# Kernel optimization log

Measured on AMD Instinct MI355X. Metric: run time of the kernel, lower is better.

Reference implementation:

```python
import jax, jax.numpy as jnp
import numpy as np

D_MODEL = 1024
D_STATE = 16
D_CONV = 4
EXPAND = 2
D_INNER = EXPAND * D_MODEL          # 2048
DT_RANK = (D_MODEL + 15) // 16      # 64
BSZ, T0, H0, W0 = 4, 8, 16, 16
SEQLEN = T0 * H0 * W0               # 2048
N_BANDS = 8


def setup_inputs() -> dict:
    key = jax.random.key(0)
    ks = jax.random.split(key, 8)
    hidden_states = jax.random.normal(ks[0], (BSZ, SEQLEN, D_MODEL), jnp.float32)
    in_proj_w = jax.random.normal(ks[1], (2 * D_INNER, D_MODEL), jnp.float32) * (D_MODEL ** -0.5)
    conv_w = jax.random.normal(ks[2], (D_INNER, 1, D_CONV), jnp.float32) * (D_CONV ** -0.5)
    conv_b = jnp.zeros((D_INNER,), jnp.float32)
    x_proj_w = jax.random.normal(ks[3], (DT_RANK + 2 * D_STATE, D_INNER), jnp.float32) * (D_INNER ** -0.5)
    dt_std = DT_RANK ** -0.5
    dt_proj_w = jax.random.uniform(ks[4], (D_INNER, DT_RANK), jnp.float32, -dt_std, dt_std)
    # inverse-softplus init of dt bias, as in the torch module
    dt = jnp.exp(jax.random.uniform(ks[5], (D_INNER,), jnp.float32)
                 * (np.log(0.1) - np.log(0.001)) + np.log(0.001))
    dt = jnp.clip(dt, 1e-4, None)
    dt_proj_b = dt + jnp.log(-jnp.expm1(-dt))
    A_log = jnp.log(jnp.tile(jnp.arange(1, D_STATE + 1, dtype=jnp.float32)[None, :], (D_INNER, 1)))
    D_param = jnp.ones((D_INNER,), jnp.float32)
    out_proj_w = jax.random.normal(ks[6], (D_MODEL, D_INNER), jnp.float32) * (D_INNER ** -0.5)
    return dict(hidden_states=hidden_states, T=T0, H=H0, W=W0,
                in_proj_w=in_proj_w, conv_w=conv_w, conv_b=conv_b,
                x_proj_w=x_proj_w, dt_proj_w=dt_proj_w, dt_proj_b=dt_proj_b,
                A_log=A_log, D=D_param, out_proj_w=out_proj_w)


def _channel_alignment(x, B, T, H, W):
    """x: (B, C, L=T*H*W) -> (align_loss scalar, features (B*T, C))."""
    C = x.shape[1]
    x4 = x.reshape(B, C, T, H, W).transpose(0, 2, 1, 3, 4).reshape(B * T, C, H, W)
    fr = jnp.fft.rfft2(x4, axes=(-2, -1))
    mag = jnp.sqrt(fr.real ** 2 + fr.imag ** 2 + 1e-8)
    mag = jnp.fft.fftshift(mag, axes=(-2, -1))
    Wr = mag.shape[-1]                      # W//2 + 1
    hg = jnp.arange(H)[:, None]
    wg = jnp.arange(Wr)[None, :]
    r = jnp.sqrt(((hg - H // 2) / H) ** 2 + ((wg - Wr // 2) / Wr) ** 2)
    masks = jnp.stack([((r >= i / N_BANDS) & (r < (i + 1) / N_BANDS)).astype(mag.dtype)
                       for i in range(N_BANDS)])          # (8, H, Wr)
    bands = jnp.einsum('bchw,khw->bck', mag, masks)        # (B*T, C, 8)
    bands = bands / (bands.sum(-1, keepdims=True) + 1e-8)
    features = bands[..., N_BANDS // 2:].sum(-1)           # (B*T, C) high-freq ratio
    fn = features / jnp.maximum(jnp.linalg.norm(features, axis=1, keepdims=True), 1e-12)
    sim = fn @ fn.T
    Bt = features.shape[0]
    loss = 1.0 - sim.sum() / (Bt * Bt)
    return loss, features


def _invert_A(A_log, features):
    """Blend A_log toward its column-flipped version, weighted by channel features."""
    A_max = A_log.max(axis=0, keepdims=True)
    A_min = A_log.min(axis=0, keepdims=True)
    A_flipped = A_max + A_min - A_log
    attention = jnp.linalg.norm(jnp.exp(A_log), axis=1)
    attention = attention / (attention.max() + 1e-8)
    f = jax.nn.softmax(jax.lax.stop_gradient(features).mean(axis=0))
    alpha = jnp.clip(f * (1.0 - attention), 0.0, 1.0)[:, None]   # (d_inner, 1)
    return (1.0 - alpha) * A_log + alpha * A_flipped


def reference(hidden_states, T, H, W, in_proj_w, conv_w, conv_b,
              x_proj_w, dt_proj_w, dt_proj_b, A_log, D, out_proj_w):
    B, L, _ = hidden_states.shape
    xz = jnp.einsum('bld,ed->bel', hidden_states, in_proj_w)      # (B, 2*d_inner, L)
    x, z = xz[:, :D_INNER], xz[:, D_INNER:]

    align_loss, features = _channel_alignment(x, B, T, H, W)
    A_log_new = _invert_A(A_log, features)
    A = -jnp.exp(A_log_new)                                       # (d_inner, d_state)

    # causal depthwise conv1d + SiLU (left pad d_conv-1 == torch pad then slice :L)
    xc = jax.lax.conv_general_dilated(x, conv_w, (1,), [(D_CONV - 1, 0)],
                                      dimension_numbers=('NCH', 'OIH', 'NCH'),
                                      feature_group_count=D_INNER)
    xc = jax.nn.silu(xc + conv_b[None, :, None])                  # (B, d_inner, L)

    x_dbl = jnp.einsum('bdl,ed->ble', xc, x_proj_w)               # (B, L, dt_rank+2N)
    dt_low = x_dbl[..., :DT_RANK]
    Bm = x_dbl[..., DT_RANK:DT_RANK + D_STATE]                    # (B, L, N)
    Cm = x_dbl[..., DT_RANK + D_STATE:]                           # (B, L, N)
    delta = jax.nn.softplus(jnp.einsum('blr,dr->bld', dt_low, dt_proj_w) + dt_proj_b)

    u = xc.transpose(0, 2, 1)                                     # (B, L, d_inner)

    def step(s, inp):
        d_t, u_t, B_t, C_t = inp                                  # (B,D),(B,D),(B,N),(B,N)
        s = s * jnp.exp(d_t[..., None] * A) + (d_t * u_t)[..., None] * B_t[:, None, :]
        y_t = jnp.einsum('bdn,bn->bd', s, C_t)
        return s, y_t

    s0 = jnp.zeros((B, D_INNER, D_STATE), delta.dtype)
    _, ys = jax.lax.scan(step, s0,
                         (delta.transpose(1, 0, 2), u.transpose(1, 0, 2),
                          Bm.transpose(1, 0, 2), Cm.transpose(1, 0, 2)))
    y = ys.transpose(1, 0, 2)                                     # (B, L, d_inner)
    y = y + u * D
    y = y * jax.nn.silu(z.transpose(0, 2, 1))
    out = jnp.einsum('bld,ed->ble', y, out_proj_w)                # (B, L, d_model)
    return out, align_loss
```

## Files before the change

kernel.cpp:

```cpp
#include <hip/hip_runtime.h>
#include <math.h>
#include <stdint.h>

#define LSEQ 2048
#define DM   1024
#define DI   2048
#define NC   32
#define CL   64

#define OFF_X     ((size_t)0)
#define OFF_Z     ((size_t)16777216)
#define OFF_U     ((size_t)33554432)
#define OFF_S     ((size_t)50331648)
#define OFF_CS    (OFF_S)
#define OFF_SDT   (OFF_S + 4194304)
#define OFF_XDBL  (OFF_S + 4456448)
#define OFF_FEAT  (OFF_S + 5242880)
#define OFF_AWS   (OFF_S + 5308448)
#define OFF_B1    ((size_t)58720256)

__device__ __forceinline__ float silu_(float x) { return x / (1.f + __expf(-x)); }
__device__ __forceinline__ float softplus_(float x) {
  return fmaxf(x, 0.f) + log1pf(__expf(-fabsf(x)));
}
__device__ __forceinline__ unsigned short f2bf(float x) {
  unsigned int u = __float_as_uint(x);
  u += 0x7fffu + ((u >> 16) & 1u);
  return (unsigned short)(u >> 16);
}
__device__ __forceinline__ float bf2f(unsigned short h) {
  return __uint_as_float(((unsigned int)h) << 16);
}

typedef __attribute__((ext_vector_type(8))) short bf16x8;
typedef __attribute__((ext_vector_type(4))) float f32x4;

__device__ __forceinline__ void gl2lds16(const void* g, void* l) {
  __builtin_amdgcn_global_load_lds(
      (const __attribute__((address_space(1))) unsigned int*)(uintptr_t)g,
      (__attribute__((address_space(3))) unsigned int*)(uintptr_t)l,
      16, 0, 0);
}

#define BARRIER_()                                   \
  do {                                               \
    asm volatile("" ::: "memory");                   \
    __builtin_amdgcn_s_barrier();                    \
    asm volatile("" ::: "memory");                   \
  } while (0)

__global__ __launch_bounds__(256) void split2_w(
    const float* __restrict__ a, unsigned short* __restrict__ oa, int ksa,
    size_t na4,
    const float* __restrict__ b, unsigned short* __restrict__ ob, int ksb)
{
  size_t i4 = ((size_t)blockIdx.x << 8) + threadIdx.x;
  const float* src; unsigned short* dst; int ks;
  if (i4 < na4) { src = a; dst = oa; ks = ksa; }
  else          { src = b; dst = ob; ks = ksb; i4 -= na4; }
  const size_t flat = i4 << 2;
  const int K = 1 << ks;
  const size_t row = flat >> ks;
  const int k = (int)(flat & (size_t)(K - 1));
  float4 v = *(const float4*)(src + flat);
  float f[4] = {v.x, v.y, v.z, v.w};
  unsigned short h[4], lo[4];
#pragma unroll
  for (int c = 0; c < 4; ++c) { h[c] = f2bf(f[c]); lo[c] = f2bf(f[c] - bf2f(h[c])); }
  unsigned short* o = dst + (row << (ks + 1)) + k;
  *(uint2*)(o)     = make_uint2((unsigned)h[0]  | ((unsigned)h[1]  << 16),
                                (unsigned)h[2]  | ((unsigned)h[3]  << 16));
  *(uint2*)(o + K) = make_uint2((unsigned)lo[0] | ((unsigned)lo[1] << 16),
                                (unsigned)lo[2] | ((unsigned)lo[3] << 16));
}

template <int NPASS, int MH, int NH>
__device__ __forceinline__ void phase_mfma(
    const unsigned short* __restrict__ shc, f32x4 (&acc)[8][4],
    int wm, int wn, int lm, int roff)
{
  bf16x8 aH[4], bH[2], aL[4], bL[2];
#pragma unroll
  for (int ii = 0; ii < 4; ++ii) {
    const int ar = (wm + (MH * 4 + ii) * 16 + lm) * 32 + roff;
    aH[ii] = *(const bf16x8*)(shc + ar);
    if constexpr (NPASS > 1) aL[ii] = *(const bf16x8*)(shc + 2 * 8192 + ar);
  }
#pragma unroll
  for (int jj = 0; jj < 2; ++jj) {
    const int br = (wn + (NH * 2 + jj) * 16 + lm) * 32 + roff;
    bH[jj] = *(const bf16x8*)(shc + 8192 + br);
    if constexpr (NPASS > 1) bL[jj] = *(const bf16x8*)(shc + 3 * 8192 + br);
  }
  __builtin_amdgcn_s_setprio(1);
#pragma unroll
  for (int ii = 0; ii < 4; ++ii)
#pragma unroll
    for (int jj = 0; jj < 2; ++jj) {
      const int i = MH * 4 + ii, j = NH * 2 + jj;
      acc[i][j] = __builtin_amdgcn_mfma_f32_16x16x32_bf16(aH[ii], bH[jj], acc[i][j], 0, 0, 0);
      if constexpr (NPASS > 1) {
        acc[i][j] = __builtin_amdgcn_mfma_f32_16x16x32_bf16(aH[ii], bL[jj], acc[i][j], 0, 0, 0);
        acc[i][j] = __builtin_amdgcn_mfma_f32_16x16x32_bf16(aL[ii], bH[jj], acc[i][j], 0, 0, 0);
      }
    }
  __builtin_amdgcn_s_setprio(0);
}

template <int NPASS>
__global__ __launch_bounds__(512, 2) void gemm_8ph(
    const unsigned short* __restrict__ Ap, const unsigned short* __restrict__ Bp,
    float* __restrict__ C, int K, int ldc)
{
  constexpr int NTEN = (NPASS > 1) ? 4 : 2;
  __shared__ unsigned short sh[2][NTEN][256 * 32];
  const int tid = threadIdx.x;
  const int bn = blockIdx.x << 8;
  const int bm = blockIdx.y << 8;
  const int K2 = K * 2;
  const int wave = tid >> 6, lane = tid & 63;
  const int wm = (wave >> 2) << 7;
  const int wn = (wave & 3) << 6;
  const int lm = lane & 15, quad = lane >> 4;
  const int roff = ((quad ^ ((lm >> 1) & 3)) << 3);

  const int r0 = tid >> 2;
  const int kq = (((tid & 3) ^ ((r0 >> 1) & 3)) << 3);
  const unsigned short* a0 = Ap + (size_t)(bm + r0) * K2 + kq;
  const unsigned short* a1 = a0 + (size_t)128 * K2;
  const unsigned short* b0 = Bp + (size_t)(bn + r0) * K2 + kq;
  const unsigned short* b1 = b0 + (size_t)128 * K2;
  const int ls0 = tid * 8, ls1 = 4096 + tid * 8;

  f32x4 acc[8][4] = {};
  const int NT = K >> 5;

  {
    unsigned short* s = &sh[0][0][0];
    gl2lds16(a0, s + ls0);
    gl2lds16(a1, s + ls1);
    if constexpr (NPASS > 1) {
      gl2lds16(a0 + K, s + 2 * 8192 + ls0);
      gl2lds16(a1 + K, s + 2 * 8192 + ls1);
    }
    gl2lds16(b0, s + 8192 + ls0);
    gl2lds16(b1, s + 8192 + ls1);
    if constexpr (NPASS > 1) {
      gl2lds16(b0 + K, s + 3 * 8192 + ls0);
      gl2lds16(b1 + K, s + 3 * 8192 + ls1);
    }
  }

  for (int t = 0; t < NT - 1; ++t) {
    const unsigned short* cur = &sh[t & 1][0][0];
    unsigned short* nxt = &sh[(t + 1) & 1][0][0];
    const int kn = (t + 1) << 5;

    gl2lds16(a0 + kn, nxt + ls0);
    gl2lds16(a1 + kn, nxt + ls1);
    if constexpr (NPASS > 1) {
      gl2lds16(a0 + K + kn, nxt + 2 * 8192 + ls0);
      gl2lds16(a1 + K + kn, nxt + 2 * 8192 + ls1);
      asm volatile("s_waitcnt vmcnt(4)" ::: "memory");
    } else {
      asm volatile("s_waitcnt vmcnt(2)" ::: "memory");
    }
    BARRIER_();
    phase_mfma<NPASS, 0, 0>(cur, acc, wm, wn, lm, roff);
    BARRIER_();
    gl2lds16(b0 + kn, nxt + 8192 + ls0);
    gl2lds16(b1 + kn, nxt + 8192 + ls1);
    if constexpr (NPASS > 1) {
      gl2lds16(b0 + K + kn, nxt + 3 * 8192 + ls0);
      gl2lds16(b1 + K + kn, nxt + 3 * 8192 + ls1);
    }
    phase_mfma<NPASS, 0, 1>(cur, acc, wm, wn, lm, roff);
    BARRIER_();
    phase_mfma<NPASS, 1, 0>(cur, acc, wm, wn, lm, roff);
    BARRIER_();
    phase_mfma<NPASS, 1, 1>(cur, acc, wm, wn, lm, roff);
    BARRIER_();
  }

  {
    const unsigned short* cur = &sh[(NT - 1) & 1][0][0];
    asm volatile("s_waitcnt vmcnt(0)" ::: "memory");
    BARRIER_();
    phase_mfma<NPASS, 0, 0>(cur, acc, wm, wn, lm, roff);
    BARRIER_();
    phase_mfma<NPASS, 0, 1>(cur, acc, wm, wn, lm, roff);
    BARRIER_();
    phase_mfma<NPASS, 1, 0>(cur, acc, wm, wn, lm, roff);
    BARRIER_();
    phase_mfma<NPASS, 1, 1>(cur, acc, wm, wn, lm, roff);
  }

#pragma unroll
  for (int i = 0; i < 8; ++i) {
    const int m = bm + wm + i * 16 + quad * 4;
#pragma unroll
    for (int j = 0; j < 4; ++j) {
      const int n = bn + wn + j * 16 + lm;
#pragma unroll
      for (int r = 0; r < 4; ++r)
        C[(size_t)(m + r) * ldc + n] = acc[i][j][r];
    }
  }
}

template <int MH>
__device__ __forceinline__ void phaseM8(
    const unsigned short* __restrict__ ah, const unsigned short* __restrict__ al,
    const unsigned short* __restrict__ bh, const unsigned short* __restrict__ bl,
    f32x4 (&acc)[8][2], int wm, int wn, int lm, int roff)
{
  bf16x8 aH[4], aL[4], bH[2], bL[2];
#pragma unroll
  for (int ii = 0; ii < 4; ++ii) {
    const int ar = (wm + (MH * 4 + ii) * 16 + lm) * 32 + roff;
    aH[ii] = *(const bf16x8*)(ah + ar);
    aL[ii] = *(const bf16x8*)(al + ar);
  }
#pragma unroll
  for (int jj = 0; jj < 2; ++jj) {
    const int br = (wn + jj * 16 + lm) * 32 + roff;
    bH[jj] = *(const bf16x8*)(bh + br);
    bL[jj] = *(const bf16x8*)(bl + br);
  }
  __builtin_amdgcn_s_setprio(1);
#pragma unroll
  for (int ii = 0; ii < 4; ++ii)
#pragma unroll
    for (int jj = 0; jj < 2; ++jj) {
      const int i = MH * 4 + ii;
      acc[i][jj] = __builtin_amdgcn_mfma_f32_16x16x32_bf16(aH[ii], bH[jj], acc[i][jj], 0, 0, 0);
      acc[i][jj] = __builtin_amdgcn_mfma_f32_16x16x32_bf16(aH[ii], bL[jj], acc[i][jj], 0, 0, 0);
      acc[i][jj] = __builtin_amdgcn_mfma_f32_16x16x32_bf16(aL[ii], bH[jj], acc[i][jj], 0, 0, 0);
    }
  __builtin_amdgcn_s_setprio(0);
}

__global__ __launch_bounds__(512, 2) void gemm8_8ph(
    const unsigned int* __restrict__ Ay,
    const unsigned short* __restrict__ Bp,
    float* __restrict__ C)
{
  constexpr int K = 2048, K2 = 4096, ldc = 1024, NT = 64;
  __shared__ unsigned short AHs[2][256 * 32];
  __shared__ unsigned short ALs[2][256 * 32];
  __shared__ unsigned short BHs[2][128 * 32];
  __shared__ unsigned short BLs[2][128 * 32];
  const int tid = threadIdx.x;
  const int bn = blockIdx.x << 7;
  const int bm = blockIdx.y << 8;
  const int wave = tid >> 6, lane = tid & 63;
  const int wm = (wave >> 2) << 7;
  const int wn = (wave & 3) << 5;
  const int lm = lane & 15, quad = lane >> 4;
  const int roff = ((quad ^ ((lm >> 1) & 3)) << 3);

  const int ra = tid >> 1;
  const int g0 = (tid & 1) << 1;
  const int aswz = (ra >> 1) & 3;
  const int sa0 = (ra * 32) + ((g0 ^ aswz) << 3);
  const int sa1 = (ra * 32) + (((g0 + 1) ^ aswz) << 3);
  const unsigned int* ag = Ay + (size_t)(bm + ra) * K + (g0 << 3);

  const int rb = tid >> 2;
  const int kqb = (((tid & 3) ^ ((rb >> 1) & 3)) << 3);
  const unsigned short* bg = Bp + (size_t)(bn + rb) * K2 + kqb;
  const int lsb = tid * 8;

  f32x4 acc[8][2] = {};
  uint4 r0a, r0b, r0c, r0d, r1a, r1b, r1c, r1d;

#define LOADA_(d0, d1, d2, d3, kn) do {                                   \
    const uint4* p_ = (const uint4*)(ag + (kn));                          \
    d0 = p_[0]; d1 = p_[1]; d2 = p_[2]; d3 = p_[3]; } while (0)
#define WRITEA_(bufi, w0, w1, w2, w3) do {                                \
    unsigned h0 = (w0.x & 0xffffu) | (w0.y << 16);                        \
    unsigned h1 = (w0.z & 0xffffu) | (w0.w << 16);                        \
    unsigned h2 = (w1.x & 0xffffu) | (w1.y << 16);                        \
    unsigned h3 = (w1.z & 0xffffu) | (w1.w << 16);                        \
    unsigned h4 = (w2.x & 0xffffu) | (w2.y << 16);                        \
    unsigned h5 = (w2.z & 0xffffu) | (w2.w << 16);                        \
    unsigned h6 = (w3.x & 0xffffu) | (w3.y << 16);                        \
    unsigned h7 = (w3.z & 0xffffu) | (w3.w << 16);                        \
    unsigned l0 = (w0.x >> 16) | (w0.y & 0xffff0000u);                    \
    unsigned l1 = (w0.z >> 16) | (w0.w & 0xffff0000u);                    \
    unsigned l2 = (w1.x >> 16) | (w1.y & 0xffff0000u);                    \
    unsigned l3 = (w1.z >> 16) | (w1.w & 0xffff0000u);                    \
    unsigned l4 = (w2.x >> 16) | (w2.y & 0xffff0000u);                    \
    unsigned l5 = (w2.z >> 16) | (w2.w & 0xffff0000u);                    \
    unsigned l6 = (w3.x >> 16) | (w3.y & 0xffff0000u);                    \
    unsigned l7 = (w3.z >> 16) | (w3.w & 0xffff0000u);                    \
    *(uint4*)&AHs[bufi][sa0] = make_uint4(h0, h1, h2, h3);                \
    *(uint4*)&AHs[bufi][sa1] = make_uint4(h4, h5, h6, h7);                \
    *(uint4*)&ALs[bufi][sa0] = make_uint4(l0, l1, l2, l3);                \
    *(uint4*)&ALs[bufi][sa1] = make_uint4(l4, l5, l6, l7); } while (0)

#define BODY_(t, Ca, Cb, Cc, Cd, Na, Nb_, Nc, Nd, cb, nb) do {            \
    LOADA_(Ca, Cb, Cc, Cd, ((t) + 2) << 5);                               \
    gl2lds16(bg + (((t) + 1) << 5),     &BHs[nb][lsb]);                   \
    gl2lds16(bg + K + (((t) + 1) << 5), &BLs[nb][lsb]);                   \
    asm volatile("s_waitcnt vmcnt(6)" ::: "memory");                      \
    BARRIER_();                                                           \
    phaseM8<0>(AHs[cb], ALs[cb], BHs[cb], BLs[cb], acc, wm, wn, lm, roff);\
    BARRIER_();                                                           \
    WRITEA_(nb, Na, Nb_, Nc, Nd);                                         \
    phaseM8<1>(AHs[cb], ALs[cb], BHs[cb], BLs[cb], acc, wm, wn, lm, roff);\
    asm volatile("s_waitcnt lgkmcnt(0)" ::: "memory");                    \
    BARRIER_();                                                           \
  } while (0)

  LOADA_(r0a, r0b, r0c, r0d, 0);
  gl2lds16(bg,     &BHs[0][lsb]);
  gl2lds16(bg + K, &BLs[0][lsb]);
  LOADA_(r1a, r1b, r1c, r1d, 32);
  asm volatile("s_waitcnt vmcnt(4)" ::: "memory");
  WRITEA_(0, r0a, r0b, r0c, r0d);
  asm volatile("s_waitcnt lgkmcnt(0)" ::: "memory");
  BARRIER_();

  for (int t = 0; t + 3 < NT; t += 2) {
    BODY_(t,     r0a, r0b, r0c, r0d, r1a, r1b, r1c, r1d, 0, 1);
    BODY_(t + 1, r1a, r1b, r1c, r1d, r0a, r0b, r0c, r0d, 1, 0);
  }

  gl2lds16(bg + ((NT - 1) << 5),     &BHs[1][lsb]);
  gl2lds16(bg + K + ((NT - 1) << 5), &BLs[1][lsb]);
  asm volatile("s_waitcnt vmcnt(2)" ::: "memory");
  BARRIER_();
  phaseM8<0>(AHs[0], ALs[0], BHs[0], BLs[0], acc, wm, wn, lm, roff);
  BARRIER_();
  WRITEA_(1, r1a, r1b, r1c, r1d);
  phaseM8<1>(AHs[0], ALs[0], BHs[0], BLs[0], acc, wm, wn, lm, roff);
  asm volatile("s_waitcnt lgkmcnt(0)" ::: "memory");
  BARRIER_();
  asm volatile("s_waitcnt vmcnt(0)" ::: "memory");
  BARRIER_();
  phaseM8<0>(AHs[1], ALs[1], BHs[1], BLs[1], acc, wm, wn, lm, roff);
  BARRIER_();
  phaseM8<1>(AHs[1], ALs[1], BHs[1], BLs[1], acc, wm, wn, lm, roff);

#undef LOADA_
#undef WRITEA_
#undef BODY_

#pragma unroll
  for (int i = 0; i < 8; ++i) {
    const int m = bm + wm + i * 16 + quad * 4;
#pragma unroll
    for (int j = 0; j < 2; ++j) {
      const int n = bn + wn + j * 16 + lm;
#pragma unroll
      for (int r = 0; r < 4; ++r)
        C[(size_t)(m + r) * ldc + n] = acc[i][j][r];
    }
  }
}

template <int EPI>
__global__ __launch_bounds__(256) void gemm_nt(
    const float* __restrict__ A, int lda,
    const float* __restrict__ B, int ldb,
    float* __restrict__ C, int ldc,
    int N, int K, const float* __restrict__ bias, size_t cseg)
{
  __shared__ float As[16][68];
  __shared__ float Bs[16][68];
  const int tid = threadIdx.x;
  const int bm = blockIdx.y << 6;
  const int bn = blockIdx.x << 6;
  const int kz = blockIdx.z;
  A += (size_t)kz * K;
  B += (size_t)kz * K;
  C += (size_t)kz * cseg;
  const int lr = tid >> 2;
  const int lk = (tid & 3) << 2;
  const int tx = tid & 15, ty = tid >> 4;

  float acc[4][4];
#pragma unroll
  for (int i = 0; i < 4; ++i)
#pragma unroll
    for (int j = 0; j < 4; ++j) acc[i][j] = 0.f;

  const float* Apt = A + (size_t)(bm + lr) * lda + lk;
  const float* Bpt = B + (size_t)(bn + lr) * ldb + lk;
  const bool bv = (bn + lr) < N;

  for (int k0 = 0; k0 < K; k0 += 16) {
    float4 a4 = *(const float4*)(Apt + k0);
    float4 b4 = bv ? *(const float4*)(Bpt + k0) : make_float4(0.f, 0.f, 0.f, 0.f);
    __syncthreads();
    As[lk + 0][lr] = a4.x; As[lk + 1][lr] = a4.y;
    As[lk + 2][lr] = a4.z; As[lk + 3][lr] = a4.w;
    Bs[lk + 0][lr] = b4.x; Bs[lk + 1][lr] = b4.y;
    Bs[lk + 2][lr] = b4.z; Bs[lk + 3][lr] = b4.w;
    __syncthreads();
#pragma unroll
    for (int k = 0; k < 16; ++k) {
      const float4 av = *(const float4*)(&As[k][ty << 2]);
      const float4 bw = *(const float4*)(&Bs[k][tx << 2]);
      float a4r[4] = {av.x, av.y, av.z, av.w};
      float b4r[4] = {bw.x, bw.y, bw.z, bw.w};
#pragma unroll
      for (int i = 0; i < 4; ++i)
#pragma unroll
        for (int j = 0; j < 4; ++j)
          acc[i][j] = fmaf(a4r[i], b4r[j], acc[i][j]);
    }
  }

  const int m = bm + (ty << 2);
  const int n = bn + (tx << 2);
#pragma unroll
  for (int i = 0; i < 4; ++i) {
    float v[4] = {acc[i][0], acc[i][1], acc[i][2], acc[i][3]};
    if (EPI == 1) {
#pragma unroll
      for (int j = 0; j < 4; ++j)
        if (n + j < N) v[j] = softplus_(v[j] + bias[n + j]);
    }
    if (n + 3 < N) {
      *(float4*)(C + (size_t)(m + i) * ldc + n) = make_float4(v[0], v[1], v[2], v[3]);
    } else {
#pragma unroll
      for (int j = 0; j < 4; ++j)
        if (n + j < N) C[(size_t)(m + i) * ldc + n + j] = v[j];
    }
  }
}

__global__ __launch_bounds__(256) void reduce4(
    const float* __restrict__ P, float* __restrict__ O, size_t seg)
{
  const size_t i = ((size_t)blockIdx.x << 8) + threadIdx.x;
  float4 a = ((const float4*)P)[i];
  float4 b = ((const float4*)(P + seg))[i];
  float4 c = ((const float4*)(P + 2 * seg))[i];
  float4 d = ((const float4*)(P + 3 * seg))[i];
  ((float4*)O)[i] = make_float4(a.x + b.x + c.x + d.x,
                                a.y + b.y + c.y + d.y,
                                a.z + b.z + c.z + d.z,
                                a.w + b.w + c.w + d.w);
}

__global__ __launch_bounds__(256) void feat_kernel(
    const float* __restrict__ X, float* __restrict__ features)
{
  __shared__ float xin[256][17];
  __shared__ float Rf[16 * 315];
  __shared__ float tc[16], ts[16];
  __shared__ float part2[16][16][2];

  const int tid = threadIdx.x;
  const int frame = blockIdx.x >> 7;
  const int cg = blockIdx.x & 127;
  const int b = frame >> 3, t = frame & 7;
  const int c0 = cg << 4;

  if (tid < 16) {
    float ang = 0.39269908169872414f * (float)tid;
    tc[tid] = cosf(ang);
    ts[tid] = sinf(ang);
  }
  const float* xb = X + ((size_t)(b * LSEQ + t * 256) << 11) + c0;
  for (int i = tid; i < 256 * 16; i += 256) {
    int hw = i >> 4, ci = i & 15;
    xin[hw][ci] = xb[((size_t)hw << 11) + ci];
  }
  __syncthreads();

  {
    const int ci = tid & 15, h = tid >> 4;
    float re[9], im[9];
#pragma unroll
    for (int kw = 0; kw < 9; ++kw) { re[kw] = 0.f; im[kw] = 0.f; }
#pragma unroll
    for (int w = 0; w < 16; ++w) {
      float x = xin[(h << 4) + w][ci];
#pragma unroll
      for (int kw = 0; kw < 9; ++kw) {
        int ph = (kw * w) & 15;
        re[kw] = fmaf(x, tc[ph], re[kw]);
        im[kw] = fmaf(-x, ts[ph], im[kw]);
      }
    }
#pragma unroll
    for (int kw = 0; kw < 9; ++kw) {
      Rf[ci * 315 + kw * 35 + 2 * h]     = re[kw];
      Rf[ci * 315 + kw * 35 + 2 * h + 1] = im[kw];
    }
  }
  __syncthreads();

  {
    const int ci = tid & 15, kh = tid >> 4;
    float ut = 0.f, tt = 0.f;
    for (int kw = 0; kw < 9; ++kw) {
      float fre = 0.f, fim = 0.f;
#pragma unroll
      for (int h = 0; h < 16; ++h) {
        int ph = (kh * h) & 15;
        float c = tc[ph], s = ts[ph];
        float rr = Rf[ci * 315 + kw * 35 + 2 * h];
        float ri = Rf[ci * 315 + kw * 35 + 2 * h + 1];
        fre += rr * c + ri * s;
        fim += ri * c - rr * s;
      }
      float mag = sqrtf(fre * fre + fim * fim + 1e-8f);
      int sh = (kh + 8) & 15;
      int sw2 = kw + 4; if (sw2 >= 9) sw2 -= 9;
      float dh = (float)(sh - 8) / 16.0f;
      float dw = (float)(sw2 - 4) / 9.0f;
      tt += mag;
      if (dh * dh + dw * dw >= 0.25f) ut += mag;
    }
    part2[ci][kh][0] = ut;
    part2[ci][kh][1] = tt;
  }
  __syncthreads();

  if (tid < 16) {
    float ut = 0.f, tt = 0.f;
    for (int kh = 0; kh < 16; ++kh) { ut += part2[tid][kh][0]; tt += part2[tid][kh][1]; }
    features[frame * DI + c0 + tid] = ut / (tt + 1e-8f);
  }
}

__global__ __launch_bounds__(256) void alpha_kernel(
    const float* __restrict__ feats, const float* __restrict__ A_log,
    float* __restrict__ Aws, float* __restrict__ loss_out)
{
  __shared__ float red[256];
  __shared__ float invn[32];
  __shared__ float PT[32][257];
  __shared__ float AM[256][17];
  __shared__ float sAmax[16], sAmin[16];
  const int tid = threadIdx.x;

  float pn[32];
#pragma unroll
  for (int i = 0; i < 32; ++i) pn[i] = 0.f;
  float md[8];
#pragma unroll
  for (int j = 0; j < 8; ++j) md[j] = 0.f;
  for (int i = 0; i < 32; ++i) {
#pragma unroll
    for (int j = 0; j < 8; ++j) {
      float v = feats[(i << 11) + tid + (j << 8)];
      pn[i] = fmaf(v, v, pn[i]);
      md[j] += v;
    }
  }
#pragma unroll
  for (int j = 0; j < 8; ++j) md[j] *= (1.f / 32.f);
#pragma unroll
  for (int i = 0; i < 32; ++i) PT[i][tid] = pn[i];
  __syncthreads();
  if (tid < 32) {
    float s = 0.f;
    for (int k = 0; k < 256; ++k) s += PT[tid][k];
    invn[tid] = 1.f / fmaxf(sqrtf(s), 1e-12f);
  }
  __syncthreads();

  float gsq = 0.f;
#pragma unroll
  for (int j = 0; j < 8; ++j) {
    float gd = 0.f;
    for (int i = 0; i < 32; ++i)
      gd = fmaf(feats[(i << 11) + tid + (j << 8)], invn[i], gd);
    gsq = fmaf(gd, gd, gsq);
  }
  red[tid] = gsq; __syncthreads();
  for (int s = 128; s > 0; s >>= 1) { if (tid < s) red[tid] += red[tid + s]; __syncthreads(); }
  if (tid == 0) loss_out[0] = 1.f - red[0] * (1.f / 1024.f);
  __syncthreads();

  float lm = md[0];
#pragma unroll
  for (int j = 1; j < 8; ++j) lm = fmaxf(lm, md[j]);
  red[tid] = lm; __syncthreads();
  for (int s = 128; s > 0; s >>= 1) { if (tid < s) red[tid] = fmaxf(red[tid], red[tid + s]); __syncthreads(); }
  const float mmax = red[0]; __syncthreads();

  float p[8]; float ps = 0.f;
#pragma unroll
  for (int j = 0; j < 8; ++j) { p[j] = __expf(md[j] - mmax); ps += p[j]; }
  red[tid] = ps; __syncthreads();
  for (int s = 128; s > 0; s >>= 1) { if (tid < s) red[tid] += red[tid + s]; __syncthreads(); }
  const float psum = red[0]; __syncthreads();

  float amaxl[16], aminl[16], rn[8];
#pragma unroll
  for (int n = 0; n < 16; ++n) { amaxl[n] = -1e30f; aminl[n] = 1e30f; }
#pragma unroll
  for (int j = 0; j < 8; ++j) {
    const int d = tid + (j << 8);
    float ss = 0.f;
#pragma unroll
    for (int n = 0; n < 16; ++n) {
      float a = A_log[(d << 4) + n];
      float e = __expf(a);
      ss = fmaf(e, e, ss);
      amaxl[n] = fmaxf(amaxl[n], a);
      aminl[n] = fminf(aminl[n], a);
    }
    rn[j] = sqrtf(ss);
  }
  float rm = rn[0];
#pragma unroll
  for (int j = 1; j < 8; ++j) rm = fmaxf(rm, rn[j]);
  red[tid] = rm; __syncthreads();
  for (int s = 128; s > 0; s >>= 1) { if (tid < s) red[tid] = fmaxf(red[tid], red[tid + s]); __syncthreads(); }
  const float rnmax = red[0]; __syncthreads();

#pragma unroll
  for (int n = 0; n < 16; ++n) AM[tid][n] = amaxl[n];
  __syncthreads();
  if (tid < 16) { float m = -1e30f; for (int i = 0; i < 256; ++i) m = fmaxf(m, AM[i][tid]); sAmax[tid] = m; }
  __syncthreads();
#pragma unroll
  for (int n = 0; n < 16; ++n) AM[tid][n] = aminl[n];
  __syncthreads();
  if (tid < 16) { float m = 1e30f; for (int i = 0; i < 256; ++i) m = fminf(m, AM[i][tid]); sAmin[tid] = m; }
  __syncthreads();

  const float irn = 1.f / (rnmax + 1e-8f);
#pragma unroll
  for (int j = 0; j < 8; ++j) {
    const int d = tid + (j << 8);
    const float att = rn[j] * irn;
    const float f = p[j] / psum;
    const float alpha = fminf(fmaxf(f * (1.f - att), 0.f), 1.f);
#pragma unroll
    for (int n = 0; n < 16; ++n) {
      float a = A_log[(d << 4) + n];
      float fl = sAmax[n] + sAmin[n] - a;
      float an = (1.f - alpha) * a + alpha * fl;
      Aws[(d << 4) + n] = -__expf(an) * 1.4426950408889634f;
    }
  }
}

__global__ __launch_bounds__(256) void conv_kernel(
    const float* __restrict__ X, const float* __restrict__ cw,
    const float* __restrict__ cb, float* __restrict__ U)
{
  const size_t i4 = ((size_t)blockIdx.x << 8) + threadIdx.x;
  const int e4 = (int)(i4 & 511);
  const size_t row = i4 >> 9;
  const int l = (int)(row & 2047);
  const float* xr = X + (row << 11) + (e4 << 2);
  const float4 z4 = make_float4(0.f, 0.f, 0.f, 0.f);
  float4 x0 = *(const float4*)xr;
  float4 x1 = (l >= 1) ? *(const float4*)(xr - 2048) : z4;
  float4 x2 = (l >= 2) ? *(const float4*)(xr - 4096) : z4;
  float4 x3 = (l >= 3) ? *(const float4*)(xr - 6144) : z4;
  const float4* cwf = (const float4*)cw;
  float4 bi = *(const float4*)(cb + (e4 << 2));
  float x0a[4] = {x0.x, x0.y, x0.z, x0.w};
  float x1a[4] = {x1.x, x1.y, x1.z, x1.w};
  float x2a[4] = {x2.x, x2.y, x2.z, x2.w};
  float x3a[4] = {x3.x, x3.y, x3.z, x3.w};
  float bia[4] = {bi.x, bi.y, bi.z, bi.w};
  float o[4];
#pragma unroll
  for (int c = 0; c < 4; ++c) {
    float4 w = cwf[(e4 << 2) + c];
    float acc = bia[c];
    acc = fmaf(x3a[c], w.x, acc);
    acc = fmaf(x2a[c], w.y, acc);
    acc = fmaf(x1a[c], w.z, acc);
    acc = fmaf(x0a[c], w.w, acc);
    o[c] = silu_(acc);
  }
  *(float4*)(U + (i4 << 2)) = make_float4(o[0], o[1], o[2], o[3]);
}

__global__ __launch_bounds__(256) void scan_pass1(
    const float* __restrict__ delta, const float* __restrict__ U,
    const float* __restrict__ xdbl, const float* __restrict__ Aws,
    float* __restrict__ cs, float* __restrict__ sdt)
{
  __shared__ float blds[CL * 16];
  const int tid = threadIdx.x;
  const int dg = blockIdx.x & 7;
  const int chunk = (blockIdx.x >> 3) & 31;
  const int b = blockIdx.x >> 8;
  const int d = (dg << 8) | tid;
  const int l0 = chunk * CL;

  for (int i = tid; i < CL * 16; i += 256) {
    int l = i >> 4, j = i & 15;
    blds[i] = xdbl[(size_t)(b * LSEQ + l0 + l) * 96 + 64 + j];
  }
  __syncthreads();

  float Ar[16];
#pragma unroll
  for (int n = 0; n < 16; ++n) Ar[n] = Aws[(d << 4) + n];
  float s[16];
#pragma unroll
  for (int n = 0; n < 16; ++n) s[n] = 0.f;
  float sumdt = 0.f;

  const float* dp = delta + ((size_t)b << 22) + ((size_t)l0 << 11) + d;
  const float* up = U + ((size_t)b << 22) + ((size_t)l0 << 11) + d;

  for (int l = 0; l < CL; ++l) {
    const float dt = dp[(size_t)l << 11];
    const float u = up[(size_t)l << 11];
    sumdt += dt;
    const float du = dt * u;
    const float* bl = &blds[l << 4];
#pragma unroll
    for (int n = 0; n < 16; ++n)
      s[n] = fmaf(s[n], __builtin_amdgcn_exp2f(dt * Ar[n]), du * bl[n]);
  }

  float* csp = cs + ((((size_t)b * NC + chunk) * 2048 + d) << 4);
#pragma unroll
  for (int n = 0; n < 4; ++n)
    *(float4*)(csp + (n << 2)) = make_float4(s[4*n], s[4*n+1], s[4*n+2], s[4*n+3]);
  sdt[((size_t)b * NC + chunk) * 2048 + d] = sumdt;
}

__global__ __launch_bounds__(256) void scan_mid(
    float* __restrict__ cs, const float* __restrict__ sdt,
    const float* __restrict__ Aws)
{
  const int b = blockIdx.x >> 3;
  const int d = ((blockIdx.x & 7) << 8) | threadIdx.x;
  float Ar[16];
#pragma unroll
  for (int n = 0; n < 16; ++n) Ar[n] = Aws[(d << 4) + n];
  float si[16];
#pragma unroll
  for (int n = 0; n < 16; ++n) si[n] = 0.f;

  for (int c = 0; c < NC; ++c) {
    const size_t base = ((size_t)b * NC + c) * 2048 + d;
    float* csp = cs + (base << 4);
    float sl[16];
#pragma unroll
    for (int n = 0; n < 4; ++n) {
      float4 v = *(const float4*)(csp + (n << 2));
      sl[4*n] = v.x; sl[4*n+1] = v.y; sl[4*n+2] = v.z; sl[4*n+3] = v.w;
    }
    const float sm = sdt[base];
#pragma unroll
    for (int n = 0; n < 4; ++n)
      *(float4*)(csp + (n << 2)) = make_float4(si[4*n], si[4*n+1], si[4*n+2], si[4*n+3]);
#pragma unroll
    for (int n = 0; n < 16; ++n)
      si[n] = fmaf(si[n], __builtin_amdgcn_exp2f(sm * Ar[n]), sl[n]);
  }
}

__global__ __launch_bounds__(256) void scan_pass3(
    const float* __restrict__ delta, const float* __restrict__ Z,
    float* __restrict__ U,
    const float* __restrict__ xdbl, const float* __restrict__ Aws,
    const float* __restrict__ Dp, const float* __restrict__ cs)
{
  __shared__ float bclds[CL * 32];
  const int tid = threadIdx.x;
  const int dg = blockIdx.x & 7;
  const int chunk = (blockIdx.x >> 3) & 31;
  const int b = blockIdx.x >> 8;
  const int d = (dg << 8) | tid;
  const int l0 = chunk * CL;

  for (int i = tid; i < CL * 32; i += 256) {
    int l = i >> 5, j = i & 31;
    bclds[i] = xdbl[(size_t)(b * LSEQ + l0 + l) * 96 + 64 + j];
  }
  __syncthreads();

  float Ar[16];
#pragma unroll
  for (int n = 0; n < 16; ++n) Ar[n] = Aws[(d << 4) + n];
  const float Dd = Dp[d];

  const float* csp = cs + ((((size_t)b * NC + chunk) * 2048 + d) << 4);
  float s[16];
#pragma unroll
  for (int n = 0; n < 4; ++n) {
    float4 v = *(const float4*)(csp + (n << 2));
    s[4*n] = v.x; s[4*n+1] = v.y; s[4*n+2] = v.z; s[4*n+3] = v.w;
  }

  const float* dp = delta + ((size_t)b << 22) + ((size_t)l0 << 11) + d;
  const float* zp = Z + ((size_t)b << 22) + ((size_t)l0 << 11) + d;
  float* up = U + ((size_t)b << 22) + ((size_t)l0 << 11) + d;

  for (int l = 0; l < CL; ++l) {
    const float dt = dp[(size_t)l << 11];
    const float u = up[(size_t)l << 11];
    const float z = zp[(size_t)l << 11];
    const float du = dt * u;
    const float* bcl = &bclds[l << 5];
    float y = 0.f;
#pragma unroll
    for (int n = 0; n < 16; ++n) {
      s[n] = fmaf(s[n], __builtin_amdgcn_exp2f(dt * Ar[n]), du * bcl[n]);
      y = fmaf(s[n], bcl[16 + n], y);
    }
    const float yv = fmaf(u, Dd, y);
    const float yo = yv * silu_(z);
    const unsigned short h = f2bf(yo);
    const unsigned short lo = f2bf(yo - bf2f(h));
    ((unsigned int*)up)[(size_t)l << 11] = (unsigned)h | ((unsigned)lo << 16);
  }
}

extern "C" void kernel_launch(void* const* d_in, const int* in_sizes, int n_in,
                              void* d_out, int out_size, void* d_ws, size_t ws_size,
                              hipStream_t stream)
{
  const float* hs         = (const float*)d_in[0];
  const float* in_proj_w  = (const float*)d_in[4];
  const float* conv_w     = (const float*)d_in[5];
  const float* conv_b     = (const float*)d_in[6];
  const float* x_proj_w   = (const float*)d_in[7];
  const float* dt_proj_w  = (const float*)d_in[8];
  const float* dt_proj_b  = (const float*)d_in[9];
  const float* A_log      = (const float*)d_in[10];
  const float* Dp         = (const float*)d_in[11];
  const float* out_proj_w = (const float*)d_in[12];
  float* out = (float*)d_out;
  float* ws = (float*)d_ws;

  float* X     = ws + OFF_X;
  float* Z     = ws + OFF_Z;
  float* U     = ws + OFF_U;
  float* cs    = ws + OFF_CS;
  float* sdt   = ws + OFF_SDT;
  float* xdbl  = ws + OFF_XDBL;
  float* feats = ws + OFF_FEAT;
  float* Aws   = ws + OFF_AWS;
  unsigned short* A1s = (unsigned short*)(ws + OFF_S);
  unsigned short* B1s = (unsigned short*)(ws + OFF_B1);
  unsigned short* B2s = (unsigned short*)(ws + OFF_B1);

  const dim3 blk(256);

  split2_w<<<12288, blk, 0, stream>>>(hs, A1s, 10, (size_t)2097152,
                                      in_proj_w, B1s, 10);
  gemm_8ph<3><<<dim3(8, 32), dim3(512), 0, stream>>>(A1s, B1s, X, 1024, 2048);
  gemm_8ph<1><<<dim3(8, 32), dim3(512), 0, stream>>>(A1s, B1s + (size_t)2048 * 2048, Z, 1024, 2048);
  feat_kernel<<<4096, blk, 0, stream>>>(X, feats);
  conv_kernel<<<16384, blk, 0, stream>>>(X, conv_w, conv_b, U);
  split2_w<<<2048, blk, 0, stream>>>(out_proj_w, B2s, 11, (size_t)524288,
                                     out_proj_w, B2s, 11);
  alpha_kernel<<<1, blk, 0, stream>>>(feats, A_log, Aws, out + 8388608);
  gemm_nt<0><<<dim3(2, 128, 4), blk, 0, stream>>>(U, DI, x_proj_w, DI, cs, 96, 96, 512, nullptr, (size_t)786432);
  reduce4<<<768, blk, 0, stream>>>(cs, xdbl, (size_t)786432);
  gemm_nt<1><<<dim3(32, 128, 1), blk, 0, stream>>>(xdbl, 96, dt_proj_w, 64, X, DI, DI, 64, dt_proj_b, 0);
  scan_pass1<<<1024, blk, 0, stream>>>(X, U, xdbl, Aws, cs, sdt);
  scan_mid<<<32, blk, 0, stream>>>(cs, sdt, Aws);
  scan_pass3<<<1024, blk, 0, stream>>>(X, Z, U, xdbl, Aws, Dp, cs);
  gemm8_8ph<<<dim3(8, 32), dim3(512), 0, stream>>>((const unsigned int*)U, B2s, out);
}
```

Before: 900.2 us.

## Stage packed A tile via direct global-to-LDS loads and split hi/lo at read

```diff
diff --git a/kernel.cpp b/kernel.cpp
--- a/kernel.cpp
+++ b/kernel.cpp
@@ -209,21 +209,34 @@
 }
 
 template <int MH>
-__device__ __forceinline__ void phaseM8(
-    const unsigned short* __restrict__ ah, const unsigned short* __restrict__ al,
+__device__ __forceinline__ void phase_pk(
+    const unsigned int* __restrict__ ap,
     const unsigned short* __restrict__ bh, const unsigned short* __restrict__ bl,
-    f32x4 (&acc)[8][2], int wm, int wn, int lm, int roff)
+    f32x4 (&acc)[8][2], int wm, int wn, int lm, int quad, int roffB)
 {
   bf16x8 aH[4], aL[4], bH[2], bL[2];
 #pragma unroll
   for (int ii = 0; ii < 4; ++ii) {
-    const int ar = (wm + (MH * 4 + ii) * 16 + lm) * 32 + roff;
-    aH[ii] = *(const bf16x8*)(ah + ar);
-    aL[ii] = *(const bf16x8*)(al + ar);
+    const int r = wm + (MH * 4 + ii) * 16 + lm;
+    const int s0 = (2 * quad) ^ (r & 7);
+    const int s1 = (2 * quad + 1) ^ (r & 7);
+    const uint4 w0 = *(const uint4*)(ap + ((size_t)(r * 8 + s0) << 2));
+    const uint4 w1 = *(const uint4*)(ap + ((size_t)(r * 8 + s1) << 2));
+    union { unsigned u[4]; bf16x8 v; } ch, cl;
+    ch.u[0] = __byte_perm(w0.x, w0.y, 0x5410u);
+    ch.u[1] = __byte_perm(w0.z, w0.w, 0x5410u);
+    ch.u[2] = __byte_perm(w1.x, w1.y, 0x5410u);
+    ch.u[3] = __byte_perm(w1.z, w1.w, 0x5410u);
+    cl.u[0] = __byte_perm(w0.x, w0.y, 0x7632u);
+    cl.u[1] = __byte_perm(w0.z, w0.w, 0x7632u);
+    cl.u[2] = __byte_perm(w1.x, w1.y, 0x7632u);
+    cl.u[3] = __byte_perm(w1.z, w1.w, 0x7632u);
+    aH[ii] = ch.v;
+    aL[ii] = cl.v;
   }
 #pragma unroll
   for (int jj = 0; jj < 2; ++jj) {
-    const int br = (wn + jj * 16 + lm) * 32 + roff;
+    const int br = (wn + jj * 16 + lm) * 32 + roffB;
     bH[jj] = *(const bf16x8*)(bh + br);
     bL[jj] = *(const bf16x8*)(bl + br);
   }
@@ -240,14 +253,13 @@
   __builtin_amdgcn_s_setprio(0);
 }
 
-__global__ __launch_bounds__(512, 2) void gemm8_8ph(
+__global__ __launch_bounds__(512, 2) void gemm8_pk(
     const unsigned int* __restrict__ Ay,
     const unsigned short* __restrict__ Bp,
     float* __restrict__ C)
 {
   constexpr int K = 2048, K2 = 4096, ldc = 1024, NT = 64;
-  __shared__ unsigned short AHs[2][256 * 32];
-  __shared__ unsigned short ALs[2][256 * 32];
+  __shared__ unsigned int   APk[2][2048 * 4];
   __shared__ unsigned short BHs[2][128 * 32];
   __shared__ unsigned short BLs[2][128 * 32];
   const int tid = threadIdx.x;
@@ -257,14 +269,11 @@
   const int wm = (wave >> 2) << 7;
   const int wn = (wave & 3) << 5;
   const int lm = lane & 15, quad = lane >> 4;
-  const int roff = ((quad ^ ((lm >> 1) & 3)) << 3);
-
-  const int ra = tid >> 1;
-  const int g0 = (tid & 1) << 1;
-  const int aswz = (ra >> 1) & 3;
-  const int sa0 = (ra * 32) + ((g0 ^ aswz) << 3);
-  const int sa1 = (ra * 32) + (((g0 + 1) ^ aswz) << 3);
-  const unsigned int* ag = Ay + (size_t)(bm + ra) * K + (g0 << 3);
+  const int roffB = ((quad ^ ((lm >> 1) & 3)) << 3);
+
+  const int ar0 = tid >> 3;
+  const int au = (tid & 7) ^ (ar0 & 7);
+  const unsigned int* ag = Ay + (size_t)(bm + ar0) * K + (au << 2);
 
   const int rb = tid >> 2;
   const int kqb = (((tid & 3) ^ ((rb >> 1) & 3)) << 3);
@@ -272,80 +281,38 @@
   const int lsb = tid * 8;
 
   f32x4 acc[8][2] = {};
-  uint4 r0a, r0b, r0c, r0d, r1a, r1b, r1c, r1d;
-
-#define LOADA_(d0, d1, d2, d3, kn) do {                                   \
-    const uint4* p_ = (const uint4*)(ag + (kn));                          \
-    d0 = p_[0]; d1 = p_[1]; d2 = p_[2]; d3 = p_[3]; } while (0)
-#define WRITEA_(bufi, w0, w1, w2, w3) do {                                \
-    unsigned h0 = (w0.x & 0xffffu) | (w0.y << 16);                        \
-    unsigned h1 = (w0.z & 0xffffu) | (w0.w << 16);                        \
-    unsigned h2 = (w1.x & 0xffffu) | (w1.y << 16);                        \
-    unsigned h3 = (w1.z & 0xffffu) | (w1.w << 16);                        \
-    unsigned h4 = (w2.x & 0xffffu) | (w2.y << 16);                        \
-    unsigned h5 = (w2.z & 0xffffu) | (w2.w << 16);                        \
-    unsigned h6 = (w3.x & 0xffffu) | (w3.y << 16);                        \
-    unsigned h7 = (w3.z & 0xffffu) | (w3.w << 16);                        \
-    unsigned l0 = (w0.x >> 16) | (w0.y & 0xffff0000u);                    \
-    unsigned l1 = (w0.z >> 16) | (w0.w & 0xffff0000u);                    \
-    unsigned l2 = (w1.x >> 16) | (w1.y & 0xffff0000u);                    \
-    unsigned l3 = (w1.z >> 16) | (w1.w & 0xffff0000u);                    \
-    unsigned l4 = (w2.x >> 16) | (w2.y & 0xffff0000u);                    \
-    unsigned l5 = (w2.z >> 16) | (w2.w & 0xffff0000u);                    \
-    unsigned l6 = (w3.x >> 16) | (w3.y & 0xffff0000u);                    \
-    unsigned l7 = (w3.z >> 16) | (w3.w & 0xffff0000u);                    \
-    *(uint4*)&AHs[bufi][sa0] = make_uint4(h0, h1, h2, h3);                \
-    *(uint4*)&AHs[bufi][sa1] = make_uint4(h4, h5, h6, h7);                \
-    *(uint4*)&ALs[bufi][sa0] = make_uint4(l0, l1, l2, l3);                \
-    *(uint4*)&ALs[bufi][sa1] = make_uint4(l4, l5, l6, l7); } while (0)
-
-#define BODY_(t, Ca, Cb, Cc, Cd, Na, Nb_, Nc, Nd, cb, nb) do {            \
-    LOADA_(Ca, Cb, Cc, Cd, ((t) + 2) << 5);                               \
-    gl2lds16(bg + (((t) + 1) << 5),     &BHs[nb][lsb]);                   \
-    gl2lds16(bg + K + (((t) + 1) << 5), &BLs[nb][lsb]);                   \
-    asm volatile("s_waitcnt vmcnt(6)" ::: "memory");                      \
-    BARRIER_();                                                           \
-    phaseM8<0>(AHs[cb], ALs[cb], BHs[cb], BLs[cb], acc, wm, wn, lm, roff);\
-    BARRIER_();                                                           \
-    WRITEA_(nb, Na, Nb_, Nc, Nd);                                         \
-    phaseM8<1>(AHs[cb], ALs[cb], BHs[cb], BLs[cb], acc, wm, wn, lm, roff);\
-    asm volatile("s_waitcnt lgkmcnt(0)" ::: "memory");                    \
-    BARRIER_();                                                           \
+
+#define STAGE_(buf, kn) do {                                                   \
+    gl2lds16(ag + (kn),                  &APk[buf][((size_t)(0 * 512 + tid)) << 2]); \
+    gl2lds16(ag + (size_t)64  * K + (kn), &APk[buf][((size_t)(1 * 512 + tid)) << 2]); \
+    gl2lds16(ag + (size_t)128 * K + (kn), &APk[buf][((size_t)(2 * 512 + tid)) << 2]); \
+    gl2lds16(ag + (size_t)192 * K + (kn), &APk[buf][((size_t)(3 * 512 + tid)) << 2]); \
+    gl2lds16(bg + (kn),     &BHs[buf][lsb]);                                   \
+    gl2lds16(bg + K + (kn), &BLs[buf][lsb]);                                   \
   } while (0)
 
-  LOADA_(r0a, r0b, r0c, r0d, 0);
-  gl2lds16(bg,     &BHs[0][lsb]);
-  gl2lds16(bg + K, &BLs[0][lsb]);
-  LOADA_(r1a, r1b, r1c, r1d, 32);
-  asm volatile("s_waitcnt vmcnt(4)" ::: "memory");
-  WRITEA_(0, r0a, r0b, r0c, r0d);
-  asm volatile("s_waitcnt lgkmcnt(0)" ::: "memory");
-  BARRIER_();
-
-  for (int t = 0; t + 3 < NT; t += 2) {
-    BODY_(t,     r0a, r0b, r0c, r0d, r1a, r1b, r1c, r1d, 0, 1);
-    BODY_(t + 1, r1a, r1b, r1c, r1d, r0a, r0b, r0c, r0d, 1, 0);
-  }
-
-  gl2lds16(bg + ((NT - 1) << 5),     &BHs[1][lsb]);
-  gl2lds16(bg + K + ((NT - 1) << 5), &BLs[1][lsb]);
-  asm volatile("s_waitcnt vmcnt(2)" ::: "memory");
-  BARRIER_();
-  phaseM8<0>(AHs[0], ALs[0], BHs[0], BLs[0], acc, wm, wn, lm, roff);
-  BARRIER_();
-  WRITEA_(1, r1a, r1b, r1c, r1d);
-  phaseM8<1>(AHs[0], ALs[0], BHs[0], BLs[0], acc, wm, wn, lm, roff);
-  asm volatile("s_waitcnt lgkmcnt(0)" ::: "memory");
-  BARRIER_();
-  asm volatile("s_waitcnt vmcnt(0)" ::: "memory");
-  BARRIER_();
-  phaseM8<0>(AHs[1], ALs[1], BHs[1], BLs[1], acc, wm, wn, lm, roff);
-  BARRIER_();
-  phaseM8<1>(AHs[1], ALs[1], BHs[1], BLs[1], acc, wm, wn, lm, roff);
-
-#undef LOADA_
-#undef WRITEA_
-#undef BODY_
+  STAGE_(0, 0);
+
+  for (int t = 0; t < NT - 1; ++t) {
+    const int cb = t & 1, nb = cb ^ 1;
+    STAGE_(nb, (t + 1) << 5);
+    asm volatile("s_waitcnt vmcnt(6)" ::: "memory");
+    BARRIER_();
+    phase_pk<0>(APk[cb], BHs[cb], BLs[cb], acc, wm, wn, lm, quad, roffB);
+    BARRIER_();
+    phase_pk<1>(APk[cb], BHs[cb], BLs[cb], acc, wm, wn, lm, quad, roffB);
+    BARRIER_();
+  }
+
+  {
+    const int cb = (NT - 1) & 1;
+    asm volatile("s_waitcnt vmcnt(0)" ::: "memory");
+    BARRIER_();
+    phase_pk<0>(APk[cb], BHs[cb], BLs[cb], acc, wm, wn, lm, quad, roffB);
+    BARRIER_();
+    phase_pk<1>(APk[cb], BHs[cb], BLs[cb], acc, wm, wn, lm, quad, roffB);
+  }
+#undef STAGE_
 
 #pragma unroll
   for (int i = 0; i < 8; ++i) {
@@ -864,5 +831,5 @@
   scan_pass1<<<1024, blk, 0, stream>>>(X, U, xdbl, Aws, cs, sdt);
   scan_mid<<<32, blk, 0, stream>>>(cs, sdt, Aws);
   scan_pass3<<<1024, blk, 0, stream>>>(X, Z, U, xdbl, Aws, Dp, cs);
-  gemm8_8ph<<<dim3(8, 32), dim3(512), 0, stream>>>((const unsigned int*)U, B2s, out);
-}
+  gemm8_pk<<<dim3(8, 32), dim3(512), 0, stream>>>((const unsigned int*)U, B2s, out);
+}
```

After: 895.0 us. Within noise of the previous version (-0.6%).
